# Optimization experiments

Measured on AMD Instinct MI355X. Metric: run time of the kernel, lower is better.

The kernel has to match this reference:

```python
import jax, jax.numpy as jnp
import numpy as np

B, S, D = 1, 1024, 1024
NH, DH, DR = 8, 128, 64
DCQ, DC = 768, 256
INTER, E, TOPK = 512, 8, 2

def rmsnorm(x, w, eps=1e-6):
    return x * jax.lax.rsqrt(jnp.mean(x * x, -1, keepdims=True) + eps) * w

def lin(x, w, b):
    return x @ w.T + b

def apply_rope(x, cos, sin):
    # x: [b, s, h, d]; cos/sin: [S, d//2]; complex rotate pairs (even, odd)
    b, s, h, d = x.shape
    xr = x.reshape(b, s, h, d // 2, 2)
    x0, x1 = xr[..., 0], xr[..., 1]
    c = cos[None, :s, None, :]
    sn = sin[None, :s, None, :]
    return jnp.stack([x0 * c - x1 * sn, x0 * sn + x1 * c], -1).reshape(b, s, h, d)

def setup_inputs():
    keys = iter(jax.random.split(jax.random.key(0), 64))
    def nrm(*shape):
        return jax.random.normal(next(keys), shape, jnp.float32) * 0.02
    theta = 1.0 / (10000.0 ** (jnp.arange(0, DR, 2, dtype=jnp.float32) / DR))
    ang = jnp.arange(S, dtype=jnp.float32)[:, None] * theta[None, :]
    return dict(
        h=jax.random.normal(next(keys), (B, S, D), jnp.float32),
        freqs_cos=jnp.cos(ang), freqs_sin=jnp.sin(ang),
        mask=jnp.triu(jnp.ones((S, S), bool), 1),
        attn_norm_w=jnp.ones(D), ffn_norm_w=jnp.ones(D),
        wq_down=nrm(DCQ, D), bq_down=jnp.zeros(DCQ), q_norm_w=jnp.ones(DCQ),
        wqc=nrm(NH * DH, DCQ), bqc=jnp.zeros(NH * DH),
        wqr=nrm(NH * DR, DCQ), bqr=jnp.zeros(NH * DR),
        wkr=nrm(DR, D), bkr=jnp.zeros(DR), kr_norm_w=jnp.ones(DR),
        wkv_down=nrm(DC, D), bkv_down=jnp.zeros(DC), kv_norm_w=jnp.ones(DC),
        wkc=nrm(NH * DH, DC), bkc=jnp.zeros(NH * DH),
        wvc=nrm(NH * DH, DC), bvc=jnp.zeros(NH * DH),
        wo=nrm(D, NH * DH), bo=jnp.zeros(D),
        sw1=nrm(INTER, D), sb1=jnp.zeros(INTER), sw2=nrm(D, INTER), sb2=jnp.zeros(D),
        sw3=nrm(INTER, D), sb3=jnp.zeros(INTER),
        ew1=nrm(E, INTER, D), eb1=jnp.zeros((E, INTER)), ew2=nrm(E, D, INTER), eb2=jnp.zeros((E, D)),
        ew3=nrm(E, INTER, D), eb3=jnp.zeros((E, INTER)),
        centroids=jax.random.normal(next(keys), (E, D), jnp.float32), biases=jnp.zeros(E),
    )

def _forward(h, freqs_cos, freqs_sin, mask, attn_norm_w, ffn_norm_w, wq_down, bq_down, q_norm_w, wqc, bqc, wqr, bqr, wkr, bkr, kr_norm_w, wkv_down, bkv_down, kv_norm_w, wkc, bkc, wvc, bvc, wo, bo, sw1, sb1, sw2, sb2, sw3, sb3, ew1, eb1, ew2, eb2, ew3, eb3, centroids, biases):
    b, s, _ = h.shape
    # --- pre-norm MLA attention ---
    x = rmsnorm(h, attn_norm_w)
    cQ = rmsnorm(lin(x, wq_down, bq_down), q_norm_w)
    qR = apply_rope(lin(cQ, wqr, bqr).reshape(b, s, NH, DR), freqs_cos, freqs_sin)
    qC = lin(cQ, wqc, bqc).reshape(b, s, NH, DH)
    q = jnp.concatenate([qC, qR], -1)                      # [b,s,NH,DH+DR]
    kR = apply_rope(rmsnorm(lin(x, wkr, bkr), kr_norm_w).reshape(b, s, 1, DR), freqs_cos, freqs_sin)
    cKV = rmsnorm(lin(x, wkv_down, bkv_down), kv_norm_w)
    kC = lin(cKV, wkc, bkc).reshape(b, s, NH, DH)
    vC = lin(cKV, wvc, bvc).reshape(b, s, NH, DH)
    k = jnp.concatenate([jnp.broadcast_to(kR, (b, s, NH, DR)), kC], -1)  # source order: [kR, kC]
    scores = jnp.einsum('bqhd,bkhd->bhqk', q, k) / jnp.sqrt(jnp.float32(DH + DR))
    scores = jnp.where(mask[None, None], jnp.finfo(scores.dtype).min, scores)
    attw = jax.nn.softmax(scores, -1)                      # dropout in eval mode = identity
    attn = jnp.einsum('bhqk,bkhd->bqhd', attw, vC).reshape(b, s, NH * DH)
    x1 = h + lin(attn, wo, bo)
    # --- pre-norm MoE FFN ---
    y = rmsnorm(x1, ffn_norm_w)
    shared = lin(jax.nn.silu(lin(y, sw1, sb1)) * lin(y, sw3, sb3), sw2, sb2)  # mean over 1 shared expert
    affinity = jax.nn.sigmoid(y @ centroids.T)             # [b,s,E]
    _, topi = jax.lax.top_k(affinity + biases, TOPK)
    gates = jax.nn.softmax(jnp.take_along_axis(affinity, topi, -1), -1)      # [b,s,TOPK]
    combine = (jax.nn.one_hot(topi, E, dtype=y.dtype) * gates[..., None]).sum(-2)  # [b,s,E]
    h1 = jax.nn.silu(jnp.einsum('bsd,eid->bsei', y, ew1) + eb1) * (jnp.einsum('bsd,eid->bsei', y, ew3) + eb3)
    out_e = jnp.einsum('bsei,edi->bsed', h1, ew2) + eb2
    routed = (out_e * combine[..., None]).sum(2)
    return x1 + shared + routed

def reference(h, freqs_cos, freqs_sin, mask, attn_norm_w, ffn_norm_w, wq_down, bq_down, q_norm_w, wqc, bqc, wqr, bqr, wkr, bkr, kr_norm_w, wkv_down, bkv_down, kv_norm_w, wkc, bkc, wvc, bvc, wo, bo, sw1, sb1, sw2, sb2, sw3, sb3, ew1, eb1, ew2, eb2, ew3, eb3, centroids, biases):
    return _forward(h, freqs_cos, freqs_sin, mask, attn_norm_w, ffn_norm_w, wq_down, bq_down, q_norm_w, wqc, bqc, wqr, bqr, wkr, bkr, kr_norm_w, wkv_down, bkv_down, kv_norm_w, wkc, bkc, wvc, bvc, wo, bo, sw1, sb1, sw2, sb2, sw3, sb3, ew1, eb1, ew2, eb2, ew3, eb3, centroids, biases)
```

## Files before the change

### kernel.cpp

```cpp
#include <hip/hip_runtime.h>

typedef unsigned short u16;
typedef __attribute__((ext_vector_type(8))) short short8;
typedef __attribute__((ext_vector_type(4))) float f32x4;

__device__ __forceinline__ float b2f(u16 u) { return __uint_as_float(((unsigned)u) << 16); }
__device__ __forceinline__ u16 f2b(float f) {
    unsigned x = __float_as_uint(f);
    return (u16)((x + 0x7fffu + ((x >> 16) & 1u)) >> 16);
}

#define GLDS16(gp, lp) __builtin_amdgcn_global_load_lds( \
    (const __attribute__((address_space(1))) void*)(gp), \
    (__attribute__((address_space(3))) void*)(lp), 16, 0, 0)

struct Seg { const u16* W; const float* bias; void* C; int ldc; int epi; int bx0; int aidx; };
struct GArgs {
    const u16* A[2]; int lda[2]; int K[2];
    Seg seg[4]; int nseg;
    const float* res;
    float* dst2;
};

__launch_bounds__(256)
__global__ void mgemm4(GArgs ga)
{
    __shared__ u16 As[8192];
    __shared__ u16 Bs[4096];
    int bx = blockIdx.x, by = blockIdx.y;
    int si = 0;
#pragma unroll
    for (int i = 1; i < 4; i++)
        if (i < ga.nseg && bx >= ga.seg[i].bx0) si = i;
    const u16* Wp = ga.seg[si].W;
    const float* bp = ga.seg[si].bias;
    void* Cp = ga.seg[si].C;
    const int ldco = ga.seg[si].ldc;
    const int epi = ga.seg[si].epi;
    const int ai = ga.seg[si].aidx;
    const u16* Ap = ga.A[ai];
    const int lda = ga.lda[ai], K = ga.K[ai];
    const int col0 = (bx - ga.seg[si].bx0) * 64;
    const int row0 = by * 128;

    int tid = threadIdx.x;
    int lane = tid & 63, w = tid >> 6;
    int r0 = (w << 4) + (lane >> 2), kc8 = (lane & 3) << 3;
    const u16* ga0 = Ap + (size_t)(row0 + r0) * lda + kc8;
    const u16* ga1 = Ap + (size_t)(row0 + r0 + 64) * lda + kc8;
    const u16* gb0 = Wp + (size_t)(col0 + r0) * lda + kc8;
    u16* lA = As + (w << 9);
    u16* lB = Bs + (w << 9);

    int wrow = w << 5;
    int fm = lane & 15, fq = lane >> 4;
    f32x4 acc[2][4] = {};

    for (int k0 = 0; k0 < K; k0 += 64) {
        GLDS16(ga0 + k0, lA);
        GLDS16(ga0 + k0 + 32, lA + 4096);
        GLDS16(ga1 + k0, lA + 2048);
        GLDS16(ga1 + k0 + 32, lA + 2048 + 4096);
        GLDS16(gb0 + k0, lB);
        GLDS16(gb0 + k0 + 32, lB + 2048);
        __syncthreads();
#pragma unroll
        for (int ks = 0; ks < 2; ks++) {
            short8 af[2], bf[4];
#pragma unroll
            for (int mt = 0; mt < 2; mt++)
                af[mt] = *(const short8*)(As + ks * 4096 + (wrow + (mt << 4) + fm) * 32 + fq * 8);
#pragma unroll
            for (int nt = 0; nt < 4; nt++)
                bf[nt] = *(const short8*)(Bs + ks * 2048 + ((nt << 4) + fm) * 32 + fq * 8);
#pragma unroll
            for (int mt = 0; mt < 2; mt++)
#pragma unroll
                for (int nt = 0; nt < 4; nt++)
                    acc[mt][nt] = __builtin_amdgcn_mfma_f32_16x16x32_bf16(af[mt], bf[nt], acc[mt][nt], 0, 0, 0);
        }
        __syncthreads();
    }

#pragma unroll
    for (int mt = 0; mt < 2; mt++) {
        int rbase = row0 + wrow + (mt << 4) + (fq << 2);
#pragma unroll
        for (int nt = 0; nt < 4; nt++) {
            int c = col0 + (nt << 4) + fm;
            float bcol = bp[c];
#pragma unroll
            for (int reg = 0; reg < 4; reg++) {
                int r = rbase + reg;
                float v = acc[mt][nt][reg] + bcol;
                if (epi == 3)
                    ((u16*)Cp)[(size_t)r * ldco + c] = f2b(v);
                else if (epi == 1) {
                    float o = v + ga.res[(size_t)r * ldco + c];
                    ((float*)Cp)[(size_t)r * ldco + c] = o;
                    if (ga.dst2) ga.dst2[(size_t)r * ldco + c] = o;
                } else
                    ((float*)Cp)[(size_t)r * ldco + c] = v;
            }
        }
    }
}

__launch_bounds__(256)
__global__ void mega_glu(const u16* __restrict__ Y16,
                         const u16* __restrict__ sw1, const float* __restrict__ sb1,
                         const u16* __restrict__ sw3, const float* __restrict__ sb3,
                         const u16* __restrict__ ew1, const float* __restrict__ eb1,
                         const u16* __restrict__ ew3, const float* __restrict__ eb3,
                         u16* __restrict__ Ub, u16* __restrict__ Vb,
                         const int* __restrict__ lists, const int* __restrict__ counts)
{
    __shared__ u16 As[8192];
    __shared__ u16 Bs[4096];
    int bx = blockIdx.x, by = blockIdx.y, z = blockIdx.z;
    bool w3 = bx >= 8;
    int col0 = (w3 ? bx - 8 : bx) * 64;
    int cnt = 1024; const int* list = nullptr;
    const u16* Wp; const float* bp;
    if (z == 0) {
        Wp = w3 ? sw3 : sw1; bp = w3 ? sb3 : sb1;
    } else {
        int e = z - 1; cnt = counts[e]; list = lists + (e << 10);
        Wp = (w3 ? ew3 : ew1) + (size_t)e * 512 * 1024;
        bp = (w3 ? eb3 : eb1) + e * 512;
    }
    int row0 = by * 128;
    if (row0 >= cnt) return;
    u16* Cp = (w3 ? Vb : Ub) + (size_t)z * 524288;

    int tid = threadIdx.x, lane = tid & 63, w = tid >> 6;
    int r0 = (w << 4) + (lane >> 2), kc8 = (lane & 3) << 3;
    int ar0 = row0 + r0, ar1 = row0 + r0 + 64;
    if (z > 0) {
        ar0 = list[ar0 < cnt ? ar0 : cnt - 1];
        ar1 = list[ar1 < cnt ? ar1 : cnt - 1];
    }
    const u16* ga0 = Y16 + (size_t)ar0 * 1024 + kc8;
    const u16* ga1 = Y16 + (size_t)ar1 * 1024 + kc8;
    const u16* gb0 = Wp + (size_t)(col0 + r0) * 1024 + kc8;
    u16* lA = As + (w << 9);
    u16* lB = Bs + (w << 9);

    int wrow = w << 5, fm = lane & 15, fq = lane >> 4;
    f32x4 acc[2][4] = {};

    for (int k0 = 0; k0 < 1024; k0 += 64) {
        GLDS16(ga0 + k0, lA);
        GLDS16(ga0 + k0 + 32, lA + 4096);
        GLDS16(ga1 + k0, lA + 2048);
        GLDS16(ga1 + k0 + 32, lA + 2048 + 4096);
        GLDS16(gb0 + k0, lB);
        GLDS16(gb0 + k0 + 32, lB + 2048);
        __syncthreads();
#pragma unroll
        for (int ks = 0; ks < 2; ks++) {
            short8 af[2], bf[4];
#pragma unroll
            for (int mt = 0; mt < 2; mt++)
                af[mt] = *(const short8*)(As + ks * 4096 + (wrow + (mt << 4) + fm) * 32 + fq * 8);
#pragma unroll
            for (int nt = 0; nt < 4; nt++)
                bf[nt] = *(const short8*)(Bs + ks * 2048 + ((nt << 4) + fm) * 32 + fq * 8);
#pragma unroll
            for (int mt = 0; mt < 2; mt++)
#pragma unroll
                for (int nt = 0; nt < 4; nt++)
                    acc[mt][nt] = __builtin_amdgcn_mfma_f32_16x16x32_bf16(af[mt], bf[nt], acc[mt][nt], 0, 0, 0);
        }
        __syncthreads();
    }

#pragma unroll
    for (int mt = 0; mt < 2; mt++) {
        int rbase = row0 + wrow + (mt << 4) + (fq << 2);
#pragma unroll
        for (int nt = 0; nt < 4; nt++) {
            int c = col0 + (nt << 4) + fm;
            float bcol = bp[c];
#pragma unroll
            for (int reg = 0; reg < 4; reg++) {
                int r = rbase + reg;
                if (r >= cnt) continue;
                Cp[(size_t)r * 512 + c] = f2b(acc[mt][nt][reg] + bcol);
            }
        }
    }
}

__launch_bounds__(256)
__global__ void mega_down(const u16* __restrict__ Ub, const u16* __restrict__ Vb,
                          const u16* __restrict__ sw2, const float* __restrict__ sb2,
                          const u16* __restrict__ ew2, const float* __restrict__ eb2,
                          float* __restrict__ out,
                          const int* __restrict__ lists, const float* __restrict__ glist,
                          const int* __restrict__ counts)
{
    __shared__ u16 Us[8192];
    __shared__ u16 Vs[8192];
    __shared__ u16 Bs[4096];
    int bx = blockIdx.x, by = blockIdx.y, z = blockIdx.z;
    int cnt = 1024; const int* list = nullptr; const float* gl = nullptr;
    const u16* Wp; const float* bp;
    if (z == 0) { Wp = sw2; bp = sb2; }
    else {
        int e = z - 1;
        cnt = counts[e]; list = lists + (e << 10); gl = glist + (e << 10);
        Wp = ew2 + (size_t)e * 1024 * 512; bp = eb2 + e * 1024;
    }
    int row0 = by * 128;
    if (row0 >= cnt) return;
    const u16* Ap = Ub + (size_t)z * 524288;
    const u16* Vp = Vb + (size_t)z * 524288;
    int col0 = bx * 64;

    int tid = threadIdx.x, lane = tid & 63, w = tid >> 6;
    int r0 = (w << 4) + (lane >> 2), kc8 = (lane & 3) << 3;
    const u16* gu0 = Ap + (size_t)(row0 + r0) * 512 + kc8;
    const u16* gu1 = Ap + (size_t)(row0 + r0 + 64) * 512 + kc8;
    const u16* gv0 = Vp + (size_t)(row0 + r0) * 512 + kc8;
    const u16* gv1 = Vp + (size_t)(row0 + r0 + 64) * 512 + kc8;
    const u16* gb0 = Wp + (size_t)(col0 + r0) * 512 + kc8;
    u16* lU = Us + (w << 9);
    u16* lV = Vs + (w << 9);
    u16* lB = Bs + (w << 9);

    int wrow = w << 5, fm = lane & 15, fq = lane >> 4;
    f32x4 acc[2][4] = {};

    for (int k0 = 0; k0 < 512; k0 += 64) {
        GLDS16(gu0 + k0, lU);        GLDS16(gu0 + k0 + 32, lU + 4096);
        GLDS16(gu1 + k0, lU + 2048); GLDS16(gu1 + k0 + 32, lU + 2048 + 4096);
        GLDS16(gv0 + k0, lV);        GLDS16(gv0 + k0 + 32, lV + 4096);
        GLDS16(gv1 + k0, lV + 2048); GLDS16(gv1 + k0 + 32, lV + 2048 + 4096);
        GLDS16(gb0 + k0, lB);        GLDS16(gb0 + k0 + 32, lB + 2048);
        __syncthreads();
#pragma unroll
        for (int ks = 0; ks < 2; ks++) {
            short8 gf[2], bf[4];
#pragma unroll
            for (int mt = 0; mt < 2; mt++) {
                int off = ks * 4096 + (wrow + (mt << 4) + fm) * 32 + fq * 8;
                short8 u8 = *(const short8*)(Us + off);
                short8 v8 = *(const short8*)(Vs + off);
#pragma unroll
                for (int i = 0; i < 8; i++) {
                    float u = b2f((u16)u8[i]), v = b2f((u16)v8[i]);
                    gf[mt][i] = (short)f2b(u / (1.f + __expf(-u)) * v);
                }
            }
#pragma unroll
            for (int nt = 0; nt < 4; nt++)
                bf[nt] = *(const short8*)(Bs + ks * 2048 + ((nt << 4) + fm) * 32 + fq * 8);
#pragma unroll
            for (int mt = 0; mt < 2; mt++)
#pragma unroll
                for (int nt = 0; nt < 4; nt++)
                    acc[mt][nt] = __builtin_amdgcn_mfma_f32_16x16x32_bf16(gf[mt], bf[nt], acc[mt][nt], 0, 0, 0);
        }
        __syncthreads();
    }

#pragma unroll
    for (int mt = 0; mt < 2; mt++) {
        int rbase = row0 + wrow + (mt << 4) + (fq << 2);
#pragma unroll
        for (int nt = 0; nt < 4; nt++) {
            int c = col0 + (nt << 4) + fm;
            float bcol = bp[c];
#pragma unroll
            for (int reg = 0; reg < 4; reg++) {
                int r = rbase + reg;
                int tok; float g;
                if (z == 0) { tok = r; g = 1.f; }
                else { if (r >= cnt) continue; tok = list[r]; g = gl[r]; }
                atomicAdd(&out[(size_t)tok * 1024 + c], g * (acc[mt][nt][reg] + bcol));
            }
        }
    }
}

__launch_bounds__(256)
__global__ void attn_mfma(const u16* __restrict__ Qp, const u16* __restrict__ Kp,
                          const u16* __restrict__ VT, u16* __restrict__ O)
{
    const int qt = blockIdx.x, h = blockIdx.y;
    const int q0 = qt * 64;
    const int tid = threadIdx.x;
    const int lane = tid & 63, w = tid >> 6;
    const int fm = lane & 15, fq = lane >> 4;

    __shared__ u16 Ks[2 * 12288];
    __shared__ u16 Vs[4 * 4096];
    __shared__ u16 Ps[4 * 2048];

    const u16* qrow = Qp + ((size_t)h * 1024 + q0 + w * 16 + fm) * 192;
    short8 qf[6];
#pragma unroll
    for (int c = 0; c < 6; c++)
        qf[c] = *(const short8*)(qrow + c * 32 + fq * 8);

    const u16* Kb = Kp + (size_t)h * 1024 * 192;
    const u16* Vb = VT + (size_t)h * 128 * 1024;

    float m_i[4], l_i[4];
#pragma unroll
    for (int r = 0; r < 4; r++) { m_i[r] = -1e30f; l_i[r] = 0.f; }
    f32x4 accO[8] = {};
    const float scale = 0.07216878364870323f;
    const int nkt = (qt >> 1) + 1;
    const int rbase = w * 16 + fq * 4;

    for (int kt = 0; kt < nkt; ++kt) {
        const int kt0 = kt * 128;
#pragma unroll
        for (int half = 0; half < 2; half++) {
            const int o = kt0 + half * 64;
#pragma unroll
            for (int i = 0; i < 6; i++) {
                int idx = w + 4 * i;
                int c = idx >> 2, k4 = idx & 3;
                const u16* g = Kb + (size_t)(o + k4 * 16 + (lane >> 2)) * 192 + c * 32 + (lane & 3) * 8;
                GLDS16(g, Ks + half * 12288 + c * 2048 + k4 * 512 + lane * 8);
            }
#pragma unroll
            for (int i = 0; i < 4; i++) {
                int idx = w + 4 * i;
                int kc = idx >> 3, k8 = idx & 7;
                const u16* g = Vb + (size_t)(k8 * 16 + (lane >> 2)) * 1024 + o + kc * 32 + (lane & 3) * 8;
                GLDS16(g, Vs + (half * 2 + kc) * 4096 + k8 * 512 + lane * 8);
            }
        }
        __syncthreads();
        f32x4 sacc[8];
#pragma unroll
        for (int nt = 0; nt < 8; nt++) {
            sacc[nt] = (f32x4){0.f, 0.f, 0.f, 0.f};
#pragma unroll
            for (int c = 0; c < 6; c++) {
                short8 kf = *(const short8*)(Ks + (nt >> 2) * 12288 + c * 2048 + ((nt & 3) * 16 + fm) * 32 + fq * 8);
                sacc[nt] = __builtin_amdgcn_mfma_f32_16x16x32_bf16(qf[c], kf, sacc[nt], 0, 0, 0);
            }
        }
        float pv[8][4], rmax[4];
#pragma unroll
        for (int reg = 0; reg < 4; reg++) {
            int q = q0 + rbase + reg;
            float mx = -1e30f;
#pragma unroll
            for (int nt = 0; nt < 8; nt++) {
                int gk = kt0 + nt * 16 + fm;
                float s = sacc[nt][reg] * scale;
                if (gk > q) s = -1e30f;
                pv[nt][reg] = s;
                mx = fmaxf(mx, s);
            }
            rmax[reg] = mx;
        }
#pragma unroll
        for (int m = 1; m < 16; m <<= 1)
#pragma unroll
            for (int reg = 0; reg < 4; reg++)
                rmax[reg] = fmaxf(rmax[reg], __shfl_xor(rmax[reg], m));
        float alpha[4], rsum[4];
#pragma unroll
        for (int reg = 0; reg < 4; reg++) {
            float mn = fmaxf(m_i[reg], rmax[reg]);
            alpha[reg] = __expf(m_i[reg] - mn);
            m_i[reg] = mn;
            float s = 0.f;
#pragma unroll
            for (int nt = 0; nt < 8; nt++) {
                float p = __expf(pv[nt][reg] - mn);
                pv[nt][reg] = p;
                s += p;
            }
            rsum[reg] = s;
        }
#pragma unroll
        for (int m = 1; m < 16; m <<= 1)
#pragma unroll
            for (int reg = 0; reg < 4; reg++)
                rsum[reg] += __shfl_xor(rsum[reg], m);
#pragma unroll
        for (int reg = 0; reg < 4; reg++)
            l_i[reg] = l_i[reg] * alpha[reg] + rsum[reg];
#pragma unroll
        for (int nt = 0; nt < 8; nt++)
#pragma unroll
            for (int reg = 0; reg < 4; reg++)
                Ps[w * 2048 + (nt >> 1) * 512 + (fq * 4 + reg) * 32 + (nt & 1) * 16 + fm]
                    = f2b(pv[nt][reg]);
#pragma unroll
        for (int n2 = 0; n2 < 8; n2++)
#pragma unroll
            for (int reg = 0; reg < 4; reg++)
                accO[n2][reg] *= alpha[reg];
        short8 pf[4];
#pragma unroll
        for (int kc = 0; kc < 4; kc++)
            pf[kc] = *(const short8*)(Ps + w * 2048 + kc * 512 + fm * 32 + fq * 8);
#pragma unroll
        for (int n2 = 0; n2 < 8; n2++)
#pragma unroll
            for (int kc = 0; kc < 4; kc++) {
                short8 vf = *(const short8*)(Vs + kc * 4096 + (n2 * 16 + fm) * 32 + fq * 8);
                accO[n2] = __builtin_amdgcn_mfma_f32_16x16x32_bf16(pf[kc], vf, accO[n2], 0, 0, 0);
            }
        __syncthreads();
    }
#pragma unroll
    for (int reg = 0; reg < 4; reg++) {
        int row = q0 + rbase + reg;
        float inv = 1.f / l_i[reg];
#pragma unroll
        for (int n2 = 0; n2 < 8; n2++)
            O[(size_t)row * 1024 + h * 128 + n2 * 16 + fm] = f2b(accO[n2][reg] * inv);
    }
}

__launch_bounds__(256)
__global__ void rmsnorm2x(const float* __restrict__ X0, const float* __restrict__ w0,
                          u16* __restrict__ O0, int c0,
                          const float* __restrict__ X1, const float* __restrict__ w1,
                          u16* __restrict__ O1, int c1)
{
    int b = blockIdx.x, tid = threadIdx.x;
    const float* X; const float* w; u16* O; int cols; int r;
    if (b < 1024) { X = X0; w = w0; O = O0; cols = c0; r = b; }
    else          { X = X1; w = w1; O = O1; cols = c1; r = b - 1024; }
    const float* xr = X + (size_t)r * cols;
    float ss = 0.f;
    for (int j = tid; j < cols; j += 256) { float v = xr[j]; ss += v * v; }
    __shared__ float red[256];
    red[tid] = ss; __syncthreads();
    for (int st = 128; st > 0; st >>= 1) { if (tid < st) red[tid] += red[tid + st]; __syncthreads(); }
    float scale = rsqrtf(red[0] / cols + 1e-6f);
    for (int j = tid; j < cols; j += 256)
        O[(size_t)r * cols + j] = f2b(xr[j] * scale * w[j]);
}

__launch_bounds__(256)
__global__ void rmsnorm_route(const float* __restrict__ X1, const float* __restrict__ ffnw,
                              u16* __restrict__ Y16,
                              const float* __restrict__ cent, const float* __restrict__ biases,
                              int* __restrict__ counts, int* __restrict__ lists,
                              float* __restrict__ glist)
{
    __shared__ float red[256];
    int b = blockIdx.x, tid = threadIdx.x;
    if (b < 1024) {
        int r = b;
        const float* xr = X1 + (size_t)r * 1024;
        float ss = 0.f;
        for (int j = tid; j < 1024; j += 256) { float v = xr[j]; ss += v * v; }
        red[tid] = ss; __syncthreads();
        for (int st = 128; st > 0; st >>= 1) { if (tid < st) red[tid] += red[tid + st]; __syncthreads(); }
        float scale = rsqrtf(red[0] / 1024.f + 1e-6f);
        for (int j = tid; j < 1024; j += 256)
            Y16[(size_t)r * 1024 + j] = f2b(xr[j] * scale * ffnw[j]);
    } else {
        int t = b - 1024;
        const float* xr = X1 + (size_t)t * 1024;
        float ss = 0.f;
        float acc[8] = {};
        for (int j = tid; j < 1024; j += 256) {
            float x = xr[j];
            ss += x * x;
            float yp = x * ffnw[j];
#pragma unroll
            for (int e = 0; e < 8; e++) acc[e] += yp * cent[e * 1024 + j];
        }
        red[tid] = ss; __syncthreads();
        for (int st = 128; st > 0; st >>= 1) { if (tid < st) red[tid] += red[tid + st]; __syncthreads(); }
        float scale = rsqrtf(red[0] / 1024.f + 1e-6f);
        __syncthreads();
        __shared__ float aff[8];
        for (int e = 0; e < 8; e++) {
            red[tid] = acc[e]; __syncthreads();
            for (int st = 128; st > 0; st >>= 1) { if (tid < st) red[tid] += red[tid + st]; __syncthreads(); }
            if (tid == 0) aff[e] = 1.f / (1.f + expf(-red[0] * scale));
            __syncthreads();
        }
        if (tid == 0) {
            float sb[8];
#pragma unroll
            for (int e = 0; e < 8; e++) sb[e] = aff[e] + biases[e];
            int i0 = 0;
            for (int e = 1; e < 8; e++) if (sb[e] > sb[i0]) i0 = e;
            int i1 = -1;
            for (int e = 0; e < 8; e++) { if (e == i0) continue; if (i1 < 0 || sb[e] > sb[i1]) i1 = e; }
            float a0 = aff[i0], a1 = aff[i1];
            float mx = fmaxf(a0, a1);
            float e0 = expf(a0 - mx), e1 = expf(a1 - mx);
            float inv = 1.f / (e0 + e1);
            int p0 = atomicAdd(&counts[i0], 1);
            lists[i0 * 1024 + p0] = t; glist[i0 * 1024 + p0] = e0 * inv;
            int p1 = atomicAdd(&counts[i1], 1);
            lists[i1 * 1024 + p1] = t; glist[i1 * 1024 + p1] = e1 * inv;
        }
    }
}

__launch_bounds__(256)
__global__ void pack_all(const float* __restrict__ QC, const float* __restrict__ QRr,
                         const float* __restrict__ KRraw, const float* __restrict__ krw,
                         const float* __restrict__ KC,
                         const u16* __restrict__ VCb,
                         const float* __restrict__ fcos, const float* __restrict__ fsin,
                         u16* __restrict__ Qp, u16* __restrict__ Kp, u16* __restrict__ VT)
{
    __shared__ u16 Ts[64][68];
    __shared__ float kshared[64];
    int b = blockIdx.x, tid = threadIdx.x;
    if (b < 1024) {
        int s = b;
        if (tid < 64) {
            float v = KRraw[(size_t)s * 64 + tid];
            float ss = v * v;
#pragma unroll
            for (int m = 1; m < 64; m <<= 1) ss += __shfl_xor(ss, m);
            float scale = rsqrtf(ss / 64.f + 1e-6f);
            int j = tid >> 1;
            float c = fcos[s * 32 + j], sn = fsin[s * 32 + j];
            float x0 = KRraw[(size_t)s * 64 + (tid & ~1)] * scale * krw[tid & ~1];
            float x1 = KRraw[(size_t)s * 64 + (tid | 1)]  * scale * krw[tid | 1];
            kshared[tid] = (tid & 1) ? (x0 * sn + x1 * c) : (x0 * c - x1 * sn);
        }
        __syncthreads();
        for (int e = tid; e < 1536; e += 256) {
            int h = e / 192, d = e % 192;
            float q;
            if (d < 128) {
                q = QC[(size_t)s * 1024 + h * 128 + d];
            } else {
                int dd = d - 128, j = dd >> 1;
                float c = fcos[s * 32 + j], sn = fsin[s * 32 + j];
                float x0 = QRr[(size_t)s * 512 + h * 64 + (dd & ~1)];
                float x1 = QRr[(size_t)s * 512 + h * 64 + (dd | 1)];
                q = (dd & 1) ? (x0 * sn + x1 * c) : (x0 * c - x1 * sn);
            }
            Qp[((size_t)h * 1024 + s) * 192 + d] = f2b(q);
            float k = (d < 64) ? kshared[d]
                               : KC[(size_t)s * 1024 + h * 128 + d - 64];
            Kp[((size_t)h * 1024 + s) * 192 + d] = f2b(k);
        }
    } else {
        int idx = b - 1024;
        int s0 = (idx & 15) * 64, d0 = (idx >> 4) * 64;
        for (int k = 0; k < 16; k++) {
            int e = tid + k * 256, r = e >> 6, c = e & 63;
            Ts[r][c] = VCb[(size_t)(s0 + r) * 1024 + d0 + c];
        }
        __syncthreads();
        for (int k = 0; k < 16; k++) {
            int e = tid + k * 256, d = e >> 6, s = e & 63;
            VT[(size_t)(d0 + d) * 1024 + s0 + s] = Ts[s][d];
        }
    }
}

#define NCAST 4096
__launch_bounds__(256)
__global__ void fused_cast(const float* p0, const float* p1, const float* p2,
                           const float* p3, const float* p4, const float* p5,
                           const float* p6, const float* p7, const float* p8,
                           const float* p9, const float* p10, const float* p11,
                           const float* p12, const float* pkr,
                           u16* __restrict__ dst,
                           const float* __restrict__ hX, const float* __restrict__ attnw,
                           u16* __restrict__ X16)
{
    __shared__ float red[256];
    int b = blockIdx.x, tid = threadIdx.x;
    if (b < NCAST) {
        const int NQ = 18022400 / 4;
        for (int i = b * 256 + tid; i < NQ; i += NCAST * 256) {
            int e = i * 4;
            const float* s; int base;
            if      (e <   786432) { s = p0;  base = 0; }
            else if (e <  1048576) { s = p1;  base =   786432; }
            else if (e <  1835008) { s = p2;  base =  1048576; }
            else if (e <  2228224) { s = p3;  base =  1835008; }
            else if (e <  2490368) { s = p4;  base =  2228224; }
            else if (e <  2752512) { s = p5;  base =  2490368; }
            else if (e <  3801088) { s = p6;  base =  2752512; }
            else if (e <  4325376) { s = p7;  base =  3801088; }
            else if (e <  4849664) { s = p8;  base =  4325376; }
            else if (e <  5373952) { s = p9;  base =  4849664; }
            else if (e <  9568256) { s = p10; base =  5373952; }
            else if (e < 13762560) { s = p11; base =  9568256; }
            else if (e < 17956864) { s = p12; base = 13762560; }
            else                   { s = pkr; base = 17956864; }
            float4 v = *(const float4*)(s + (e - base));
            ushort4 o;
            o.x = f2b(v.x); o.y = f2b(v.y); o.z = f2b(v.z); o.w = f2b(v.w);
            *(ushort4*)(dst + e) = o;
        }
    } else {
        int r = b - NCAST;
        const float* xr = hX + (size_t)r * 1024;
        float ss = 0.f;
        for (int j = tid; j < 1024; j += 256) { float v = xr[j]; ss += v * v; }
        red[tid] = ss; __syncthreads();
        for (int st = 128; st > 0; st >>= 1) { if (tid < st) red[tid] += red[tid + st]; __syncthreads(); }
        float scale = rsqrtf(red[0] / 1024.f + 1e-6f);
        for (int j = tid; j < 1024; j += 256)
            X16[(size_t)r * 1024 + j] = f2b(xr[j] * scale * attnw[j]);
    }
}

extern "C" void kernel_launch(void* const* d_in, const int* in_sizes, int n_in,
                              void* d_out, int out_size, void* d_ws, size_t ws_size,
                              hipStream_t stream)
{
    (void)in_sizes; (void)n_in; (void)ws_size; (void)out_size;
    const float* h       = (const float*)d_in[0];
    const float* fcos    = (const float*)d_in[1];
    const float* fsin    = (const float*)d_in[2];
    const float* attn_w  = (const float*)d_in[4];
    const float* ffn_w   = (const float*)d_in[5];
    const float* wq_down = (const float*)d_in[6];
    const float* bq_down = (const float*)d_in[7];
    const float* q_norm  = (const float*)d_in[8];
    const float* wqc     = (const float*)d_in[9];
    const float* bqc     = (const float*)d_in[10];
    const float* wqr     = (const float*)d_in[11];
    const float* bqr     = (const float*)d_in[12];
    const float* wkr     = (const float*)d_in[13];
    const float* bkr     = (const float*)d_in[14];
    const float* kr_norm = (const float*)d_in[15];
    const float* wkv     = (const float*)d_in[16];
    const float* bkv     = (const float*)d_in[17];
    const float* kv_norm = (const float*)d_in[18];
    const float* wkc     = (const float*)d_in[19];
    const float* bkc     = (const float*)d_in[20];
    const float* wvc     = (const float*)d_in[21];
    const float* bvc     = (const float*)d_in[22];
    const float* wo      = (const float*)d_in[23];
    const float* bo      = (const float*)d_in[24];
    const float* sw1     = (const float*)d_in[25];
    const float* sb1     = (const float*)d_in[26];
    const float* sw2     = (const float*)d_in[27];
    const float* sb2     = (const float*)d_in[28];
    const float* sw3     = (const float*)d_in[29];
    const float* sb3     = (const float*)d_in[30];
    const float* ew1     = (const float*)d_in[31];
    const float* eb1     = (const float*)d_in[32];
    const float* ew2     = (const float*)d_in[33];
    const float* eb2     = (const float*)d_in[34];
    const float* ew3     = (const float*)d_in[35];
    const float* eb3     = (const float*)d_in[36];
    const float* cent    = (const float*)d_in[37];
    const float* biases  = (const float*)d_in[38];

    char* wsb = (char*)d_ws;
    const size_t U5 = 512 * 1024;
    u16*   X16   = (u16*)(wsb + 8 * U5);
    float* QRr   = (float*)(wsb + 12 * U5);
    float* CQraw = (float*)(wsb + 16 * U5);
    u16*   ATT16 = (u16*)(wsb + 16 * U5);
    u16*   CQ16  = (u16*)(wsb + 22 * U5);
    float* CKVraw= (float*)(wsb + 25 * U5);
    u16*   CKV16 = (u16*)(wsb + 27 * U5);
    float* KRraw = (float*)(wsb + 28 * U5);
    float* QC    = (float*)(wsb + 29 * U5);
    float* KC    = (float*)(wsb + 37 * U5);
    u16*   Vb    = (u16*)(wsb + 29 * U5);
    float* X1    = (float*)(wsb + 53 * U5);
    float* GL    = (float*)(wsb + 61 * U5);
    int*   lists = (int*)(wsb + 61 * U5 + 32 * 1024);
    int*   counts= (int*)(wsb + 61 * U5 + 64 * 1024);
    u16*   Y16   = (u16*)(wsb + 69 * U5);
    u16*   Ub    = (u16*)(wsb + 73 * U5);

    u16* wb = (u16*)(wsb + 92 * U5);
    u16 *c_wq  = wb;
    u16 *c_wkv = c_wq  + 786432;
    u16 *c_wqc = c_wkv + 262144;
    u16 *c_wqr = c_wqc + 786432;
    u16 *c_wkc = c_wqr + 393216;
    u16 *c_wvc = c_wkc + 262144;
    u16 *c_wo  = c_wvc + 262144;
    u16 *c_sw1 = c_wo  + 1048576;
    u16 *c_sw3 = c_sw1 + 524288;
    u16 *c_sw2 = c_sw3 + 524288;
    u16 *c_ew1 = c_sw2 + 524288;
    u16 *c_ew3 = c_ew1 + 4194304;
    u16 *c_ew2 = c_ew3 + 4194304;
    u16 *c_wkr = c_ew2 + 4194304;
    u16* VCb = (u16*)(wsb + 92 * U5 + 36175872);
    u16* VTp = VCb + 1048576;
    u16* Qpk = VTp + 1048576;
    u16* Kpk = Qpk + 1572864;

    fused_cast<<<NCAST + 1024, 256, 0, stream>>>(wq_down, wkv, wqc, wqr, wkc, wvc, wo,
                                                 sw1, sw3, sw2, ew1, ew3, ew2, wkr, wb,
                                                 h, attn_w, X16);

    {
        GArgs g = {};
        g.A[0] = X16; g.lda[0] = 1024; g.K[0] = 1024;
        g.seg[0] = { c_wq,  bq_down, CQraw,  768, 0, 0,  0 };
        g.seg[1] = { c_wkv, bkv,     CKVraw, 256, 0, 12, 0 };
        g.seg[2] = { c_wkr, bkr,     KRraw,  64,  0, 16, 0 };
        g.nseg = 3;
        mgemm4<<<dim3(17, 8), 256, 0, stream>>>(g);
    }
    rmsnorm2x<<<2048, 256, 0, stream>>>(CQraw, q_norm, CQ16, 768,
                                        CKVraw, kv_norm, CKV16, 256);
    {
        GArgs g = {};
        g.A[0] = CQ16;  g.lda[0] = 768; g.K[0] = 768;
        g.A[1] = CKV16; g.lda[1] = 256; g.K[1] = 256;
        g.seg[0] = { c_wqc, bqc, QC,   1024, 0, 0,  0 };
        g.seg[1] = { c_wqr, bqr, QRr,  512,  0, 16, 0 };
        g.seg[2] = { c_wkc, bkc, KC,   1024, 0, 24, 1 };
        g.seg[3] = { c_wvc, bvc, VCb,  1024, 3, 40, 1 };
        g.nseg = 4;
        mgemm4<<<dim3(56, 8), 256, 0, stream>>>(g);
    }
    pack_all<<<1280, 256, 0, stream>>>(QC, QRr, KRraw, kr_norm, KC, VCb, fcos, fsin,
                                       Qpk, Kpk, VTp);
    attn_mfma<<<dim3(16, 8), 256, 0, stream>>>(Qpk, Kpk, VTp, ATT16);
    {
        GArgs g = {};
        g.A[0] = ATT16; g.lda[0] = 1024; g.K[0] = 1024;
        g.seg[0] = { c_wo, bo, X1, 1024, 1, 0, 0 };
        g.nseg = 1; g.res = h; g.dst2 = (float*)d_out;
        mgemm4<<<dim3(16, 8), 256, 0, stream>>>(g);
    }

    hipMemsetAsync(counts, 0, 32, stream);
    rmsnorm_route<<<2048, 256, 0, stream>>>(X1, ffn_w, Y16, cent, biases,
                                            counts, lists, GL);
    mega_glu<<<dim3(16, 8, 9), 256, 0, stream>>>(Y16, c_sw1, sb1, c_sw3, sb3,
                                                 c_ew1, eb1, c_ew3, eb3,
                                                 Ub, Vb, lists, counts);
    mega_down<<<dim3(16, 8, 9), 256, 0, stream>>>(Ub, Vb, c_sw2, sb2, c_ew2, eb2,
                                                  (float*)d_out, lists, GL, counts);
}
```

Measured before the change: 420.6 us.

## Load MoE GLU and down-proj MFMA operands directly from global, dropping LDS staging

Both MoE kernels (gate/up GLU and down projection) no longer stage A/B tiles through shared memory with global_load_lds and barriers. Each lane now loads its MFMA fragments straight from global memory (L2/L1 cached), with the loop unrolled by four. This removes the LDS traffic and per-iteration __syncthreads, and frees LDS for higher occupancy. In exchange, weight fragments that other waves also need are fetched redundantly from global memory, and the loads are 16-byte strided per row rather than coalesced tiles.

```diff
diff --git a/kernel.cpp b/kernel.cpp
--- a/kernel.cpp
+++ b/kernel.cpp
@@ -115,8 +115,6 @@
                          u16* __restrict__ Ub, u16* __restrict__ Vb,
                          const int* __restrict__ lists, const int* __restrict__ counts)
 {
-    __shared__ u16 As[8192];
-    __shared__ u16 Bs[4096];
     int bx = blockIdx.x, by = blockIdx.y, z = blockIdx.z;
     bool w3 = bx >= 8;
     int col0 = (w3 ? bx - 8 : bx) * 64;
@@ -134,45 +132,32 @@
     u16* Cp = (w3 ? Vb : Ub) + (size_t)z * 524288;
 
     int tid = threadIdx.x, lane = tid & 63, w = tid >> 6;
-    int r0 = (w << 4) + (lane >> 2), kc8 = (lane & 3) << 3;
-    int ar0 = row0 + r0, ar1 = row0 + r0 + 64;
+    int wrow = w << 5, fm = lane & 15, fq = lane >> 4;
+
+    int ar0 = row0 + wrow + fm;
+    int ar1 = ar0 + 16;
     if (z > 0) {
         ar0 = list[ar0 < cnt ? ar0 : cnt - 1];
         ar1 = list[ar1 < cnt ? ar1 : cnt - 1];
     }
-    const u16* ga0 = Y16 + (size_t)ar0 * 1024 + kc8;
-    const u16* ga1 = Y16 + (size_t)ar1 * 1024 + kc8;
-    const u16* gb0 = Wp + (size_t)(col0 + r0) * 1024 + kc8;
-    u16* lA = As + (w << 9);
-    u16* lB = Bs + (w << 9);
-
-    int wrow = w << 5, fm = lane & 15, fq = lane >> 4;
+    const u16* gA0 = Y16 + (size_t)ar0 * 1024 + fq * 8;
+    const u16* gA1 = Y16 + (size_t)ar1 * 1024 + fq * 8;
+    const u16* gB[4];
+#pragma unroll
+    for (int nt = 0; nt < 4; nt++)
+        gB[nt] = Wp + (size_t)(col0 + (nt << 4) + fm) * 1024 + fq * 8;
+
     f32x4 acc[2][4] = {};
-
-    for (int k0 = 0; k0 < 1024; k0 += 64) {
-        GLDS16(ga0 + k0, lA);
-        GLDS16(ga0 + k0 + 32, lA + 4096);
-        GLDS16(ga1 + k0, lA + 2048);
-        GLDS16(ga1 + k0 + 32, lA + 2048 + 4096);
-        GLDS16(gb0 + k0, lB);
-        GLDS16(gb0 + k0 + 32, lB + 2048);
-        __syncthreads();
-#pragma unroll
-        for (int ks = 0; ks < 2; ks++) {
-            short8 af[2], bf[4];
-#pragma unroll
-            for (int mt = 0; mt < 2; mt++)
-                af[mt] = *(const short8*)(As + ks * 4096 + (wrow + (mt << 4) + fm) * 32 + fq * 8);
-#pragma unroll
-            for (int nt = 0; nt < 4; nt++)
-                bf[nt] = *(const short8*)(Bs + ks * 2048 + ((nt << 4) + fm) * 32 + fq * 8);
-#pragma unroll
-            for (int mt = 0; mt < 2; mt++)
-#pragma unroll
-                for (int nt = 0; nt < 4; nt++)
-                    acc[mt][nt] = __builtin_amdgcn_mfma_f32_16x16x32_bf16(af[mt], bf[nt], acc[mt][nt], 0, 0, 0);
-        }
-        __syncthreads();
+#pragma unroll 4
+    for (int k = 0; k < 1024; k += 32) {
+        short8 af0 = *(const short8*)(gA0 + k);
+        short8 af1 = *(const short8*)(gA1 + k);
+#pragma unroll
+        for (int nt = 0; nt < 4; nt++) {
+            short8 bf = *(const short8*)(gB[nt] + k);
+            acc[0][nt] = __builtin_amdgcn_mfma_f32_16x16x32_bf16(af0, bf, acc[0][nt], 0, 0, 0);
+            acc[1][nt] = __builtin_amdgcn_mfma_f32_16x16x32_bf16(af1, bf, acc[1][nt], 0, 0, 0);
+        }
     }
 
 #pragma unroll
@@ -200,9 +185,6 @@
                           const int* __restrict__ lists, const float* __restrict__ glist,
                           const int* __restrict__ counts)
 {
-    __shared__ u16 Us[8192];
-    __shared__ u16 Vs[8192];
-    __shared__ u16 Bs[4096];
     int bx = blockIdx.x, by = blockIdx.y, z = blockIdx.z;
     int cnt = 1024; const int* list = nullptr; const float* gl = nullptr;
     const u16* Wp; const float* bp;
@@ -219,50 +201,38 @@
     int col0 = bx * 64;
 
     int tid = threadIdx.x, lane = tid & 63, w = tid >> 6;
-    int r0 = (w << 4) + (lane >> 2), kc8 = (lane & 3) << 3;
-    const u16* gu0 = Ap + (size_t)(row0 + r0) * 512 + kc8;
-    const u16* gu1 = Ap + (size_t)(row0 + r0 + 64) * 512 + kc8;
-    const u16* gv0 = Vp + (size_t)(row0 + r0) * 512 + kc8;
-    const u16* gv1 = Vp + (size_t)(row0 + r0 + 64) * 512 + kc8;
-    const u16* gb0 = Wp + (size_t)(col0 + r0) * 512 + kc8;
-    u16* lU = Us + (w << 9);
-    u16* lV = Vs + (w << 9);
-    u16* lB = Bs + (w << 9);
-
     int wrow = w << 5, fm = lane & 15, fq = lane >> 4;
+
+    const u16* gU0 = Ap + (size_t)(row0 + wrow + fm) * 512 + fq * 8;
+    const u16* gU1 = gU0 + 16 * 512;
+    const u16* gV0 = Vp + (size_t)(row0 + wrow + fm) * 512 + fq * 8;
+    const u16* gV1 = gV0 + 16 * 512;
+    const u16* gB[4];
+#pragma unroll
+    for (int nt = 0; nt < 4; nt++)
+        gB[nt] = Wp + (size_t)(col0 + (nt << 4) + fm) * 512 + fq * 8;
+
     f32x4 acc[2][4] = {};
-
-    for (int k0 = 0; k0 < 512; k0 += 64) {
-        GLDS16(gu0 + k0, lU);        GLDS16(gu0 + k0 + 32, lU + 4096);
-        GLDS16(gu1 + k0, lU + 2048); GLDS16(gu1 + k0 + 32, lU + 2048 + 4096);
-        GLDS16(gv0 + k0, lV);        GLDS16(gv0 + k0 + 32, lV + 4096);
-        GLDS16(gv1 + k0, lV + 2048); GLDS16(gv1 + k0 + 32, lV + 2048 + 4096);
-        GLDS16(gb0 + k0, lB);        GLDS16(gb0 + k0 + 32, lB + 2048);
-        __syncthreads();
-#pragma unroll
-        for (int ks = 0; ks < 2; ks++) {
-            short8 gf[2], bf[4];
-#pragma unroll
-            for (int mt = 0; mt < 2; mt++) {
-                int off = ks * 4096 + (wrow + (mt << 4) + fm) * 32 + fq * 8;
-                short8 u8 = *(const short8*)(Us + off);
-                short8 v8 = *(const short8*)(Vs + off);
-#pragma unroll
-                for (int i = 0; i < 8; i++) {
-                    float u = b2f((u16)u8[i]), v = b2f((u16)v8[i]);
-                    gf[mt][i] = (short)f2b(u / (1.f + __expf(-u)) * v);
-                }
-            }
-#pragma unroll
-            for (int nt = 0; nt < 4; nt++)
-                bf[nt] = *(const short8*)(Bs + ks * 2048 + ((nt << 4) + fm) * 32 + fq * 8);
-#pragma unroll
-            for (int mt = 0; mt < 2; mt++)
-#pragma unroll
-                for (int nt = 0; nt < 4; nt++)
-                    acc[mt][nt] = __builtin_amdgcn_mfma_f32_16x16x32_bf16(gf[mt], bf[nt], acc[mt][nt], 0, 0, 0);
-        }
-        __syncthreads();
+#pragma unroll 4
+    for (int k = 0; k < 512; k += 32) {
+        short8 u0 = *(const short8*)(gU0 + k);
+        short8 u1 = *(const short8*)(gU1 + k);
+        short8 v0 = *(const short8*)(gV0 + k);
+        short8 v1 = *(const short8*)(gV1 + k);
+        short8 gf[2];
+#pragma unroll
+        for (int i = 0; i < 8; i++) {
+            float u = b2f((u16)u0[i]), v = b2f((u16)v0[i]);
+            gf[0][i] = (short)f2b(u / (1.f + __expf(-u)) * v);
+            u = b2f((u16)u1[i]); v = b2f((u16)v1[i]);
+            gf[1][i] = (short)f2b(u / (1.f + __expf(-u)) * v);
+        }
+#pragma unroll
+        for (int nt = 0; nt < 4; nt++) {
+            short8 bf = *(const short8*)(gB[nt] + k);
+            acc[0][nt] = __builtin_amdgcn_mfma_f32_16x16x32_bf16(gf[0], bf, acc[0][nt], 0, 0, 0);
+            acc[1][nt] = __builtin_amdgcn_mfma_f32_16x16x32_bf16(gf[1], bf, acc[1][nt], 0, 0, 0);
+        }
     }
 
 #pragma unroll
```

Result: slower. 498.9 us (+18.6%).
